# Kernel tuning notes

Measured on AMD Instinct MI355X. Metric: run time of the kernel, lower is better.

## Reference

```python
import jax, jax.numpy as jnp
import numpy as np

B, T, H, D = 1, 2048, 32, 128
Q_GROUP = 4
HKV = H // Q_GROUP
INNER = H * D
KV_INNER = HKV * D
ROPE_BASE = 10000.0
NEG = -1e30


def _rope_tables(seq_len, head_dim, dtype):
    inv_freq = 1.0 / (ROPE_BASE ** (jnp.arange(0, head_dim, 2, dtype=jnp.float32) / head_dim))
    t = jnp.arange(seq_len, dtype=jnp.float32)
    freqs = jnp.einsum('t,f->tf', t, inv_freq)          # [T, D/2]
    emb = jnp.concatenate([freqs, freqs], axis=-1)      # [T, D]
    cos = jnp.cos(emb)[None, :, None, :].astype(dtype)  # [1, T, 1, D]
    sin = jnp.sin(emb)[None, :, None, :].astype(dtype)
    return cos, sin


def _rotate(x, cos, sin):
    # x: [B, T, H, D]; split-half rotation: cat(-x2, x1)
    half = x.shape[-1] // 2
    x1, x2 = x[..., :half], x[..., half:]
    x_rot = jnp.concatenate([-x2, x1], axis=-1)
    return x * cos + x_rot * sin


def setup_inputs() -> dict:
    key = jax.random.key(0)
    ks = jax.random.split(key, 5)
    return {
        'stm': jax.random.normal(ks[0], (B, T, H, D), dtype=jnp.float32),
        'w_q': jax.random.normal(ks[1], (INNER, INNER), dtype=jnp.float32) * 0.02,
        'w_k': jax.random.normal(ks[2], (KV_INNER, INNER), dtype=jnp.float32) * 0.02,
        'w_v': jax.random.normal(ks[3], (KV_INNER, INNER), dtype=jnp.float32) * 0.02,
        'w_o': jax.random.normal(ks[4], (INNER, INNER), dtype=jnp.float32) * 0.02,
    }


def reference(stm, w_q, w_k, w_v, w_o):
    b, t, h, d = stm.shape
    x = stm.reshape(b * t, h * d)
    q = x @ w_q.T                                   # [B*T, H*D]
    k = x @ w_k.T                                   # [B*T, Hkv*D]
    v = x @ w_v.T
    # GQA repeat_interleave over query-group axis (broadcast then reshape)
    k = jnp.broadcast_to(k.reshape(b * t, HKV, 1, d), (b * t, HKV, Q_GROUP, d)).reshape(b, t, h, d)
    v = jnp.broadcast_to(v.reshape(b * t, HKV, 1, d), (b * t, HKV, Q_GROUP, d)).reshape(b, t, h, d)
    q = q.reshape(b, t, h, d)
    cos, sin = _rope_tables(t, d, stm.dtype)        # prefill: seq_start = 0
    q = _rotate(q, cos, sin)
    k = _rotate(k, cos, sin)                        # rotated k is what gets written to the KV cache
    scale = 1.0 / np.sqrt(d)
    scores = jnp.einsum('bqhd,bkhd->bhqk', q, k).astype(jnp.float32) * scale
    causal = jnp.tril(jnp.ones((t, t), dtype=jnp.float32))          # mask_w
    bias = (1.0 - causal) * NEG                                     # mask_b
    scores = scores * causal[None, None] + bias[None, None]
    attn = jax.nn.softmax(scores, axis=-1).astype(stm.dtype)
    o = jnp.einsum('bhqk,bkhd->bqhd', attn, v)
    o = o.reshape(b * t, h * d) @ w_o.T
    return o.reshape(b, t, h, d)
```

## Files before the change

kernel.cpp:

```cpp
#include <hip/hip_runtime.h>
#include <hip/hip_bf16.h>
#include <stdint.h>
#include <stddef.h>

using bf16  = __hip_bfloat16;
using v4s   = __attribute__((ext_vector_type(4))) short;
using v8s   = __attribute__((ext_vector_type(8))) short;
using f32x4 = __attribute__((ext_vector_type(4))) float;

#define MFMA_16x16x32(a, b, c) __builtin_amdgcn_mfma_f32_16x16x32_bf16((a), (b), (c), 0, 0, 0)

__device__ __forceinline__ void async_lds16(const bf16* g, bf16* l) {
  __builtin_amdgcn_global_load_lds(
      (const __attribute__((address_space(1))) void*)g,
      (__attribute__((address_space(3))) void*)l, 16, 0, 0);
}

__device__ __forceinline__ short bf16_bits(float f) {
  bf16 h = __float2bfloat16(f);
  short s;
  __builtin_memcpy(&s, &h, sizeof(s));
  return s;
}

__global__ void cvt_f32_bf16(const float* __restrict__ in, bf16* __restrict__ out,
                             int n4) {
  const int i = blockIdx.x * blockDim.x + threadIdx.x;
  if (i >= n4) return;
  const float4 f = ((const float4*)in)[i];
  v4s o;
  o[0] = bf16_bits(f.x);
  o[1] = bf16_bits(f.y);
  o[2] = bf16_bits(f.z);
  o[3] = bf16_bits(f.w);
  *(v4s*)(out + (size_t)i * 4) = o;
}

template <bool F32OUT>
__global__ __launch_bounds__(256) void gemm_bt(const bf16* __restrict__ A,
                                               const bf16* __restrict__ B,
                                               void* __restrict__ C,
                                               int M, int N, int K) {
  __shared__ bf16 As[8 * 512];
  __shared__ bf16 Bs[8 * 512];
  const int tid  = threadIdx.x;
  const int w    = tid >> 6;
  const int lane = tid & 63;
  const int quad = lane >> 4;
  const int m16  = lane & 15;
  const int tm = blockIdx.y, tn = blockIdx.x;
  const int wrow = w >> 1, wcol = w & 1;

  f32x4 acc[4][4] = {};

  const bf16* Ag0 = A + (size_t)(tm * 128 + (w * 2 + 0) * 16 + m16) * K + quad * 8;
  const bf16* Ag1 = A + (size_t)(tm * 128 + (w * 2 + 1) * 16 + m16) * K + quad * 8;
  const bf16* Bg0 = B + (size_t)(tn * 128 + (w * 2 + 0) * 16 + m16) * K + quad * 8;
  const bf16* Bg1 = B + (size_t)(tn * 128 + (w * 2 + 1) * 16 + m16) * K + quad * 8;
  bf16* As0 = &As[(w * 2 + 0) * 512];
  bf16* As1 = &As[(w * 2 + 1) * 512];
  bf16* Bs0 = &Bs[(w * 2 + 0) * 512];
  bf16* Bs1 = &Bs[(w * 2 + 1) * 512];

  for (int k0 = 0; k0 < K; k0 += 32) {
    async_lds16(Ag0 + k0, As0);
    async_lds16(Ag1 + k0, As1);
    async_lds16(Bg0 + k0, Bs0);
    async_lds16(Bg1 + k0, Bs1);
    __syncthreads();
    v8s af[4], bfv[4];
#pragma unroll
    for (int i = 0; i < 4; ++i) af[i]  = *(const v8s*)&As[(wrow * 4 + i) * 512 + lane * 8];
#pragma unroll
    for (int i = 0; i < 4; ++i) bfv[i] = *(const v8s*)&Bs[(wcol * 4 + i) * 512 + lane * 8];
#pragma unroll
    for (int mi = 0; mi < 4; ++mi)
#pragma unroll
      for (int ni = 0; ni < 4; ++ni)
        acc[mi][ni] = MFMA_16x16x32(af[mi], bfv[ni], acc[mi][ni]);
    __syncthreads();
  }
#pragma unroll
  for (int mi = 0; mi < 4; ++mi)
#pragma unroll
    for (int ni = 0; ni < 4; ++ni) {
      const int row = tm * 128 + wrow * 64 + mi * 16 + quad * 4;
      const int col = tn * 128 + wcol * 64 + ni * 16 + m16;
#pragma unroll
      for (int r = 0; r < 4; ++r) {
        if (F32OUT)
          ((float*)C)[(size_t)(row + r) * N + col] = acc[mi][ni][r];
        else
          ((bf16*)C)[(size_t)(row + r) * N + col] = __float2bfloat16(acc[mi][ni][r]);
      }
    }
}

__global__ void rope_kernel(bf16* __restrict__ qkv) {
  const int t  = blockIdx.x;
  const int hh = blockIdx.y;
  const int d  = threadIdx.x;
  const float invf = powf(10000.0f, -(float)(d & 63) * (1.0f / 64.0f));
  const float ang  = (float)t * invf;
  const float c = cosf(ang);
  const float s = sinf(ang);
  const bool isq = (hh < 32);
  bf16* ptr = qkv + (size_t)t * 6144 + (isq ? hh * 128 : 4096 + (hh - 32) * 128);
  const float x   = __bfloat162float(ptr[d]);
  const float xp  = __bfloat162float(ptr[d ^ 64]);
  __syncthreads();
  const float rot = (d < 64) ? -xp : xp;
  const float outv = (x * c + rot * s) * (isq ? 0.08838834764831845f : 1.0f);
  ptr[d] = __float2bfloat16(outv);
}

__global__ void vtrans_kernel(const bf16* __restrict__ qkv, bf16* __restrict__ vt) {
  __shared__ bf16 tile[32][34];
  const int t0 = blockIdx.x * 32, c0 = blockIdx.y * 32;
  const int tx = threadIdx.x, ty = threadIdx.y;
#pragma unroll
  for (int i = 0; i < 4; ++i)
    tile[ty + 8 * i][tx] = qkv[(size_t)(t0 + ty + 8 * i) * 6144 + 5120 + c0 + tx];
  __syncthreads();
#pragma unroll
  for (int i = 0; i < 4; ++i)
    vt[(size_t)(c0 + ty + 8 * i) * 2048 + t0 + tx] = tile[tx][ty + 8 * i];
}

__global__ __launch_bounds__(256) void attn_fused3(const bf16* __restrict__ QKV,
                                                   const bf16* __restrict__ Vt,
                                                   bf16* __restrict__ O) {
  const int qt = 15 - (int)blockIdx.x;
  const int h = blockIdx.y, hk = h >> 2;
  const int tid = threadIdx.x, w = tid >> 6, lane = tid & 63;
  const int quad = lane >> 4, m16 = lane & 15;
  __shared__ bf16 Ks[32 * 512];
  __shared__ bf16 Vs[32 * 512];
  short* Pw = (short*)Ks + w * 4096;

  v8s qf[2][4];
#pragma unroll
  for (int ni = 0; ni < 2; ++ni)
#pragma unroll
    for (int dk = 0; dk < 4; ++dk)
      qf[ni][dk] = *(const v8s*)(QKV + (size_t)(qt * 128 + w * 32 + ni * 16 + m16) * 6144 +
                                 h * 128 + dk * 32 + quad * 8);

  f32x4 acc[8][2] = {};
  float m_run[2] = {-1e30f, -1e30f}, l_run[2] = {0.f, 0.f};

  for (int kt = 0; kt <= qt; ++kt) {
    __syncthreads();
    const bf16* kg = QKV + (size_t)(kt * 128 + m16) * 6144 + 4096 + hk * 128 + w * 32 + quad * 8;
    const bf16* vg = Vt + (size_t)(hk * 128 + m16) * 2048 + kt * 128 + w * 32 + quad * 8;
#pragma unroll
    for (int mi = 0; mi < 8; ++mi) {
      async_lds16(kg + (size_t)mi * 16 * 6144, &Ks[(mi * 4 + w) * 512]);
      async_lds16(vg + (size_t)mi * 16 * 2048, &Vs[(mi * 4 + w) * 512]);
    }
    __syncthreads();
    f32x4 s[8][2];
#pragma unroll
    for (int mi = 0; mi < 8; ++mi) {
      s[mi][0] = f32x4{0.f, 0.f, 0.f, 0.f};
      s[mi][1] = f32x4{0.f, 0.f, 0.f, 0.f};
#pragma unroll
      for (int dk = 0; dk < 4; ++dk) {
        v8s af = *(const v8s*)&Ks[(mi * 4 + dk) * 512 + lane * 8];
        s[mi][0] = MFMA_16x16x32(af, qf[0][dk], s[mi][0]);
        s[mi][1] = MFMA_16x16x32(af, qf[1][dk], s[mi][1]);
      }
    }
    if (kt == qt) {
#pragma unroll
      for (int mi = 0; mi < 8; ++mi)
#pragma unroll
        for (int ni = 0; ni < 2; ++ni)
#pragma unroll
          for (int r = 0; r < 4; ++r)
            if (mi * 16 + quad * 4 + r > w * 32 + ni * 16 + m16) s[mi][ni][r] = -1e30f;
    }
#pragma unroll
    for (int ni = 0; ni < 2; ++ni) {
      float mx = -1e30f;
#pragma unroll
      for (int mi = 0; mi < 8; ++mi)
#pragma unroll
        for (int r = 0; r < 4; ++r) mx = fmaxf(mx, s[mi][ni][r]);
      mx = fmaxf(mx, __shfl_xor(mx, 16));
      mx = fmaxf(mx, __shfl_xor(mx, 32));
      const float mnew = fmaxf(m_run[ni], mx);
      const float alpha = __expf(m_run[ni] - mnew);
      m_run[ni] = mnew;
      float rs = 0.f;
#pragma unroll
      for (int mi = 0; mi < 8; ++mi)
#pragma unroll
        for (int r = 0; r < 4; ++r) {
          const float p = __expf(s[mi][ni][r] - mnew);
          s[mi][ni][r] = p;
          rs += p;
        }
      rs += __shfl_xor(rs, 16);
      rs += __shfl_xor(rs, 32);
      l_run[ni] = l_run[ni] * alpha + rs;
#pragma unroll
      for (int mi2 = 0; mi2 < 8; ++mi2)
#pragma unroll
        for (int r = 0; r < 4; ++r) acc[mi2][ni][r] *= alpha;
    }
    __syncthreads();
#pragma unroll
    for (int mi = 0; mi < 8; ++mi)
#pragma unroll
      for (int ni = 0; ni < 2; ++ni) {
        v4s p4;
#pragma unroll
        for (int r = 0; r < 4; ++r) p4[r] = bf16_bits(s[mi][ni][r]);
        const int base = (ni * 4 + (mi >> 1)) * 512 +
                         ((mi & 1) * 2 + (quad >> 1)) * 128 + m16 * 8 + (quad & 1) * 4;
        *(v4s*)&Pw[base] = p4;
      }
    asm volatile("" ::: "memory");
#pragma unroll
    for (int kp = 0; kp < 4; ++kp) {
      v8s pf0 = *(const v8s*)&Pw[(0 * 4 + kp) * 512 + lane * 8];
      v8s pf1 = *(const v8s*)&Pw[(1 * 4 + kp) * 512 + lane * 8];
#pragma unroll
      for (int mi2 = 0; mi2 < 8; ++mi2) {
        v8s vf = *(const v8s*)&Vs[(mi2 * 4 + kp) * 512 + lane * 8];
        acc[mi2][0] = MFMA_16x16x32(vf, pf0, acc[mi2][0]);
        acc[mi2][1] = MFMA_16x16x32(vf, pf1, acc[mi2][1]);
      }
    }
  }
#pragma unroll
  for (int ni = 0; ni < 2; ++ni) {
    const float rl = 1.0f / l_run[ni];
    const size_t qrow = qt * 128 + w * 32 + ni * 16 + m16;
#pragma unroll
    for (int mi2 = 0; mi2 < 8; ++mi2) {
      v4s o4;
#pragma unroll
      for (int r = 0; r < 4; ++r) o4[r] = bf16_bits(acc[mi2][ni][r] * rl);
      *(v4s*)(O + qrow * 4096 + h * 128 + mi2 * 16 + quad * 4) = o4;
    }
  }
}

extern "C" void kernel_launch(void* const* d_in, const int* in_sizes, int n_in,
                              void* d_out, int out_size, void* d_ws, size_t ws_size,
                              hipStream_t stream) {
  const float* stm = (const float*)d_in[0];
  const float* w_q = (const float*)d_in[1];
  const float* w_k = (const float*)d_in[2];
  const float* w_v = (const float*)d_in[3];
  const float* w_o = (const float*)d_in[4];
  float* out = (float*)d_out;

  const size_t M_STM = (size_t)2048 * 4096;
  const size_t M_WQ  = (size_t)4096 * 4096;
  const size_t M_WK  = (size_t)1024 * 4096;

  bf16* ws      = (bf16*)d_ws;
  bf16* wqkv_bf = ws;
  bf16* wo_bf   = ws;
  bf16* vT      = ws + M_WQ;
  bf16* stm_bf  = ws + 24 * 1024 * 1024;
  bf16* o_buf   = stm_bf;
  bf16* qkv_buf = ws + 32 * 1024 * 1024;

  cvt_f32_bf16<<<(int)(M_STM / 1024), 256, 0, stream>>>(stm, stm_bf, (int)(M_STM / 4));
  cvt_f32_bf16<<<(int)(M_WQ / 1024), 256, 0, stream>>>(w_q, wqkv_bf, (int)(M_WQ / 4));
  cvt_f32_bf16<<<(int)(M_WK / 1024), 256, 0, stream>>>(w_k, wqkv_bf + M_WQ, (int)(M_WK / 4));
  cvt_f32_bf16<<<(int)(M_WK / 1024), 256, 0, stream>>>(w_v, wqkv_bf + M_WQ + M_WK, (int)(M_WK / 4));

  gemm_bt<false><<<dim3(48, 16), 256, 0, stream>>>(stm_bf, wqkv_bf, qkv_buf, 2048, 6144, 4096);

  cvt_f32_bf16<<<(int)(M_WQ / 1024), 256, 0, stream>>>(w_o, wo_bf, (int)(M_WQ / 4));

  rope_kernel<<<dim3(2048, 40), 128, 0, stream>>>(qkv_buf);
  vtrans_kernel<<<dim3(64, 32), dim3(32, 8), 0, stream>>>(qkv_buf, vT);
  attn_fused3<<<dim3(16, 32), 256, 0, stream>>>(qkv_buf, vT, o_buf);

  gemm_bt<true><<<dim3(32, 16), 256, 0, stream>>>(o_buf, wo_bf, out, 2048, 4096, 4096);
}
```

Measured before the change: 743.8 us.

## Replace GEMM with 256x256 8-wave double-buffered pipelined kernel

Both projection GEMMs switch to a new kernel with 256x256 output tiles, 512 threads and a K step of 64. It double-buffers LDS and issues async global-to-LDS loads interleaved with MFMA phases under barriers and raised wave priority. The aim is to hide memory latency and raise per-tile reuse, replacing the old 128x128 kernel that stalled at every K step. The trade-off is far fewer blocks than CUs (192 and 128), 128KB of LDS per block and dependence on a hand-tuned waitcnt schedule.

```diff
diff --git a/kernel.cpp b/kernel.cpp
--- a/kernel.cpp
+++ b/kernel.cpp
@@ -37,55 +37,130 @@
 }
 
 template <bool F32OUT>
-__global__ __launch_bounds__(256) void gemm_bt(const bf16* __restrict__ A,
-                                               const bf16* __restrict__ B,
-                                               void* __restrict__ C,
-                                               int M, int N, int K) {
-  __shared__ bf16 As[8 * 512];
-  __shared__ bf16 Bs[8 * 512];
+__global__ __launch_bounds__(512, 2) void gemm_bt8(const bf16* __restrict__ A,
+                                                   const bf16* __restrict__ B,
+                                                   void* __restrict__ C,
+                                                   int M, int N, int K) {
+  __shared__ bf16 lds[2][64][512];
   const int tid  = threadIdx.x;
   const int w    = tid >> 6;
   const int lane = tid & 63;
   const int quad = lane >> 4;
   const int m16  = lane & 15;
+  const int wr = w >> 2, wc = w & 3;
   const int tm = blockIdx.y, tn = blockIdx.x;
-  const int wrow = w >> 1, wcol = w & 1;
-
-  f32x4 acc[4][4] = {};
-
-  const bf16* Ag0 = A + (size_t)(tm * 128 + (w * 2 + 0) * 16 + m16) * K + quad * 8;
-  const bf16* Ag1 = A + (size_t)(tm * 128 + (w * 2 + 1) * 16 + m16) * K + quad * 8;
-  const bf16* Bg0 = B + (size_t)(tn * 128 + (w * 2 + 0) * 16 + m16) * K + quad * 8;
-  const bf16* Bg1 = B + (size_t)(tn * 128 + (w * 2 + 1) * 16 + m16) * K + quad * 8;
-  bf16* As0 = &As[(w * 2 + 0) * 512];
-  bf16* As1 = &As[(w * 2 + 1) * 512];
-  bf16* Bs0 = &Bs[(w * 2 + 0) * 512];
-  bf16* Bs1 = &Bs[(w * 2 + 1) * 512];
-
-  for (int k0 = 0; k0 < K; k0 += 32) {
-    async_lds16(Ag0 + k0, As0);
-    async_lds16(Ag1 + k0, As1);
-    async_lds16(Bg0 + k0, Bs0);
-    async_lds16(Bg1 + k0, Bs1);
-    __syncthreads();
-    v8s af[4], bfv[4];
-#pragma unroll
-    for (int i = 0; i < 4; ++i) af[i]  = *(const v8s*)&As[(wrow * 4 + i) * 512 + lane * 8];
-#pragma unroll
-    for (int i = 0; i < 4; ++i) bfv[i] = *(const v8s*)&Bs[(wcol * 4 + i) * 512 + lane * 8];
+  const int NKT = K >> 6;
+
+  const bf16* Ast0 = A + (size_t)(tm * 256 + w * 16 + m16) * K + quad * 8;
+  const bf16* Ast1 = Ast0 + (size_t)128 * K;
+  const bf16* Bst0 = B + (size_t)(tn * 256 + w * 16 + m16) * K + quad * 8;
+  const bf16* Bst1 = Bst0 + (size_t)128 * K;
+
+  auto stage = [&](const bf16* g, bf16* l) {
+    async_lds16(g, l);
+    async_lds16(g + 32, l + 512);
+  };
+
+  f32x4 acc[8][4] = {};
+
+  {
+    bf16* L0 = &lds[0][0][0];
+    bf16* L1 = &lds[1][0][0];
+    stage(Bst0, L0 + (32 + w * 2) * 512);
+    stage(Bst1, L0 + (48 + w * 2) * 512);
+    stage(Ast0, L0 + (w * 2) * 512);
+    stage(Ast1, L0 + (16 + w * 2) * 512);
+    stage(Bst0 + 64, L1 + (32 + w * 2) * 512);
+    stage(Bst1 + 64, L1 + (48 + w * 2) * 512);
+    stage(Ast0 + 64, L1 + (w * 2) * 512);
+  }
+  asm volatile("s_waitcnt vmcnt(6)" ::: "memory");
+  __builtin_amdgcn_s_barrier();
+
+  for (int k = 0; k < NKT; ++k) {
+    bf16* Lc = &lds[k & 1][0][0];
+    bf16* Ln = &lds[(k & 1) ^ 1][0][0];
+    v8s af[4][2], bfv[4][2];
+#pragma unroll
+    for (int mi = 0; mi < 4; ++mi) {
+      af[mi][0] = *(const v8s*)(Lc + ((wr * 8 + mi) * 2 + 0) * 512 + lane * 8);
+      af[mi][1] = *(const v8s*)(Lc + ((wr * 8 + mi) * 2 + 1) * 512 + lane * 8);
+    }
+#pragma unroll
+    for (int ni = 0; ni < 4; ++ni) {
+      bfv[ni][0] = *(const v8s*)(Lc + (32 + (wc * 4 + ni) * 2 + 0) * 512 + lane * 8);
+      bfv[ni][1] = *(const v8s*)(Lc + (32 + (wc * 4 + ni) * 2 + 1) * 512 + lane * 8);
+    }
+    if (k + 1 < NKT) stage(Ast1 + (size_t)(k + 1) * 64, Ln + (16 + w * 2) * 512);
+    __builtin_amdgcn_s_barrier();
+    asm volatile("s_waitcnt lgkmcnt(0)" ::: "memory");
+    __builtin_amdgcn_sched_barrier(0);
+    __builtin_amdgcn_s_setprio(1);
 #pragma unroll
     for (int mi = 0; mi < 4; ++mi)
 #pragma unroll
-      for (int ni = 0; ni < 4; ++ni)
-        acc[mi][ni] = MFMA_16x16x32(af[mi], bfv[ni], acc[mi][ni]);
-    __syncthreads();
+      for (int ni = 0; ni < 2; ++ni) {
+        acc[mi][ni] = MFMA_16x16x32(af[mi][0], bfv[ni][0], acc[mi][ni]);
+        acc[mi][ni] = MFMA_16x16x32(af[mi][1], bfv[ni][1], acc[mi][ni]);
+      }
+    __builtin_amdgcn_s_setprio(0);
+    __builtin_amdgcn_s_barrier();
+    if (k + 2 < NKT) stage(Bst0 + (size_t)(k + 2) * 64, Lc + (32 + w * 2) * 512);
+    __builtin_amdgcn_s_barrier();
+    __builtin_amdgcn_s_setprio(1);
+#pragma unroll
+    for (int mi = 0; mi < 4; ++mi)
+#pragma unroll
+      for (int ni = 2; ni < 4; ++ni) {
+        acc[mi][ni] = MFMA_16x16x32(af[mi][0], bfv[ni][0], acc[mi][ni]);
+        acc[mi][ni] = MFMA_16x16x32(af[mi][1], bfv[ni][1], acc[mi][ni]);
+      }
+    __builtin_amdgcn_s_setprio(0);
+    __builtin_amdgcn_s_barrier();
+#pragma unroll
+    for (int mi = 0; mi < 4; ++mi) {
+      af[mi][0] = *(const v8s*)(Lc + ((wr * 8 + 4 + mi) * 2 + 0) * 512 + lane * 8);
+      af[mi][1] = *(const v8s*)(Lc + ((wr * 8 + 4 + mi) * 2 + 1) * 512 + lane * 8);
+    }
+    if (k + 2 < NKT) stage(Bst1 + (size_t)(k + 2) * 64, Lc + (48 + w * 2) * 512);
+    __builtin_amdgcn_s_barrier();
+    asm volatile("s_waitcnt lgkmcnt(0)" ::: "memory");
+    __builtin_amdgcn_sched_barrier(0);
+    __builtin_amdgcn_s_setprio(1);
+#pragma unroll
+    for (int mi = 0; mi < 4; ++mi)
+#pragma unroll
+      for (int ni = 0; ni < 2; ++ni) {
+        acc[4 + mi][ni] = MFMA_16x16x32(af[mi][0], bfv[ni][0], acc[4 + mi][ni]);
+        acc[4 + mi][ni] = MFMA_16x16x32(af[mi][1], bfv[ni][1], acc[4 + mi][ni]);
+      }
+    __builtin_amdgcn_s_setprio(0);
+    __builtin_amdgcn_s_barrier();
+    if (k + 2 < NKT) stage(Ast0 + (size_t)(k + 2) * 64, Lc + (w * 2) * 512);
+    if (k < NKT - 2) {
+      asm volatile("s_waitcnt vmcnt(6)" ::: "memory");
+    } else {
+      asm volatile("s_waitcnt vmcnt(0)" ::: "memory");
+    }
+    __builtin_amdgcn_s_barrier();
+    __builtin_amdgcn_s_setprio(1);
+#pragma unroll
+    for (int mi = 0; mi < 4; ++mi)
+#pragma unroll
+      for (int ni = 2; ni < 4; ++ni) {
+        acc[4 + mi][ni] = MFMA_16x16x32(af[mi][0], bfv[ni][0], acc[4 + mi][ni]);
+        acc[4 + mi][ni] = MFMA_16x16x32(af[mi][1], bfv[ni][1], acc[4 + mi][ni]);
+      }
+    __builtin_amdgcn_s_setprio(0);
+    __builtin_amdgcn_s_barrier();
   }
-#pragma unroll
-  for (int mi = 0; mi < 4; ++mi)
+
+#pragma unroll
+  for (int mi = 0; mi < 8; ++mi)
 #pragma unroll
     for (int ni = 0; ni < 4; ++ni) {
-      const int row = tm * 128 + wrow * 64 + mi * 16 + quad * 4;
-      const int col = tn * 128 + wcol * 64 + ni * 16 + m16;
+      const int row = tm * 256 + wr * 128 + mi * 16 + quad * 4;
+      const int col = tn * 256 + wc * 64 + ni * 16 + m16;
 #pragma unroll
       for (int r = 0; r < 4; ++r) {
         if (F32OUT)
@@ -275,7 +350,7 @@
   cvt_f32_bf16<<<(int)(M_WK / 1024), 256, 0, stream>>>(w_k, wqkv_bf + M_WQ, (int)(M_WK / 4));
   cvt_f32_bf16<<<(int)(M_WK / 1024), 256, 0, stream>>>(w_v, wqkv_bf + M_WQ + M_WK, (int)(M_WK / 4));
 
-  gemm_bt<false><<<dim3(48, 16), 256, 0, stream>>>(stm_bf, wqkv_bf, qkv_buf, 2048, 6144, 4096);
+  gemm_bt8<false><<<dim3(24, 8), 512, 0, stream>>>(stm_bf, wqkv_bf, qkv_buf, 2048, 6144, 4096);
 
   cvt_f32_bf16<<<(int)(M_WQ / 1024), 256, 0, stream>>>(w_o, wo_bf, (int)(M_WQ / 4));
 
@@ -283,5 +358,5 @@
   vtrans_kernel<<<dim3(64, 32), dim3(32, 8), 0, stream>>>(qkv_buf, vT);
   attn_fused3<<<dim3(16, 32), 256, 0, stream>>>(qkv_buf, vT, o_buf);
 
-  gemm_bt<true><<<dim3(32, 16), 256, 0, stream>>>(o_buf, wo_bf, out, 2048, 4096, 4096);
-}
+  gemm_bt8<true><<<dim3(16, 8), 512, 0, stream>>>(o_buf, wo_bf, out, 2048, 4096, 4096);
+}
```

Result: faster. 680.1 us (-8.6%).
